# Performance work log

Hardware: AMD Instinct MI355X
Metric: run time of the kernel (lower is better)

The kernel has to match this reference:

```python
import jax, jax.numpy as jnp
import numpy as np


def setup_inputs() -> dict:
    key = jax.random.key(0)
    k1, k2, k3, k4 = jax.random.split(key, 4)
    T = 64            # decoder_batch_len (target steps)
    B = 32            # batch_size
    V = 50257         # decoder vocab size
    L = 400           # encoder (source) length
    rows = T * B
    vocab_ds = jax.random.uniform(k1, (rows, V), dtype=jnp.float32)
    attns = jax.random.uniform(k2, (rows, L), dtype=jnp.float32)
    p_gens = jax.random.uniform(k3, (rows, 1), dtype=jnp.float32)
    sources = jax.random.randint(k4, (L, B), 0, V, dtype=jnp.int64)
    return {
        "vocab_ds": vocab_ds,
        "attns": attns,
        "p_gens": p_gens,
        "sources": sources,
        "decoder_batch_len": T,
    }


def reference(vocab_ds, attns, p_gens, sources, decoder_batch_len):
    # vocab_ds: (T*B, V), attns: (T*B, L), p_gens: (T*B, 1), sources: (L, B)
    rows, V = vocab_ds.shape
    vocab_dists = p_gens * vocab_ds                      # gated generation dist
    attn_dists = (1.0 - p_gens) * attns                  # gated copy dist
    # sources.T tiled over decoder steps -> per-row vocab ids, shape (T*B, L)
    sources_rep = jnp.tile(sources.T, (decoder_batch_len, 1))
    row_idx = jnp.arange(rows)[:, None]                  # (T*B, 1) broadcasts over L
    # torch scatter_ (overwrite semantics) of copy probs into vocab slots
    attn_dists_projected = jnp.zeros((rows, V), dtype=vocab_ds.dtype).at[
        row_idx, sources_rep
    ].set(attn_dists, mode="drop")
    final_dists = attn_dists_projected + vocab_dists
    return final_dists
```

## Files before the change

kernel.cpp:

```cpp
#include <hip/hip_runtime.h>

__global__ __launch_bounds__(256) void distgen_kernel(
    const float* __restrict__ vocab_ds,
    const float* __restrict__ attns,
    const float* __restrict__ p_gens,
    const int*   __restrict__ sources,
    float* __restrict__ out,
    int V, int L, int B)
{
    const int row = blockIdx.x;
    const int tid = threadIdx.x;
    const size_t base = (size_t)row * (size_t)V;
    const float pg = p_gens[row];

    const int mis  = (int)(base & 3);
    const int pre  = mis ? (4 - mis) : 0;
    const int preN = pre < V ? pre : V;
    for (int j = tid; j < preN; j += blockDim.x)
        out[base + j] = pg * vocab_ds[base + j];

    const int rem  = V - preN;
    const int nvec = rem >> 2;
    const float4* __restrict__ v4 = (const float4*)(vocab_ds + base + preN);
    float4* __restrict__ o4       = (float4*)(out + base + preN);
    for (int i = tid; i < nvec; i += blockDim.x) {
        float4 x = v4[i];
        x.x *= pg; x.y *= pg; x.z *= pg; x.w *= pg;
        o4[i] = x;
    }
    for (int j = preN + (nvec << 2) + tid; j < V; j += blockDim.x)
        out[base + j] = pg * vocab_ds[base + j];

    __shared__ int s_src[512];
    const int b = row % B;
    const bool use_lds = (L <= 512);
    if (use_lds) {
        for (int l = tid; l < L; l += blockDim.x)
            s_src[l] = sources[(size_t)l * B + b];
    }
    __syncthreads();

    const float gate = 1.0f - pg;
    for (int l = tid; l < L; l += blockDim.x) {
        const int v = use_lds ? s_src[l] : sources[(size_t)l * B + b];
        if (v < 0 || v >= V) continue;
        bool last = true;
        if (use_lds) {
            for (int l2 = l + 1; l2 < L; ++l2)
                if (s_src[l2] == v) { last = false; break; }
        } else {
            for (int l2 = l + 1; l2 < L; ++l2)
                if (sources[(size_t)l2 * B + b] == v) { last = false; break; }
        }
        if (last) {
            const float a = gate * attns[(size_t)row * L + l];
            out[base + v] = pg * vocab_ds[base + v] + a;
        }
    }
}

extern "C" void kernel_launch(void* const* d_in, const int* in_sizes, int n_in,
                              void* d_out, int out_size, void* d_ws, size_t ws_size,
                              hipStream_t stream) {
    const float* vocab_ds = (const float*)d_in[0];
    const float* attns    = (const float*)d_in[1];
    const float* p_gens   = (const float*)d_in[2];
    const int*   sources  = (const int*)d_in[3];
    const int rows = in_sizes[2];
    const int V    = in_sizes[0] / rows;
    const int L    = in_sizes[1] / rows;
    const int B    = in_sizes[3] / L;
    float* out = (float*)d_out;

    distgen_kernel<<<rows, 256, 0, stream>>>(vocab_ds, attns, p_gens, sources,
                                             out, V, L, B);
}
```

Before: 282.5 us.

## Precompute per-batch last-occurrence mask and split into scale and scatter kernels

Moves the O(L^2) duplicate-source search out of every row into a small mask kernel that runs once per batch column and writes the surviving vocab ids to workspace. The main work then becomes a bandwidth-bound scale kernel (4x unrolled float4 loads, nontemporal stores) followed by a light scatter kernel that overwrites the copy positions. This removes the redundant per-row (T-fold) duplicate search and the latency it adds at the end of each block. In exchange it adds two launches and a second pass over roughly L scattered output elements per row, and it keeps the old fused kernel as a fallback when workspace is too small.

```diff
diff --git a/kernel.cpp b/kernel.cpp
--- a/kernel.cpp
+++ b/kernel.cpp
@@ -1,12 +1,96 @@
 #include <hip/hip_runtime.h>
 
-__global__ __launch_bounds__(256) void distgen_kernel(
-    const float* __restrict__ vocab_ds,
-    const float* __restrict__ attns,
-    const float* __restrict__ p_gens,
-    const int*   __restrict__ sources,
-    float* __restrict__ out,
-    int V, int L, int B)
+typedef float f32x4 __attribute__((ext_vector_type(4)));
+
+#define LMAX 1024
+
+__global__ __launch_bounds__(256) void mask_kernel(
+    const int* __restrict__ sources, int* __restrict__ vlast, int L, int B)
+{
+    const int b = blockIdx.x;
+    __shared__ int s_col[LMAX];
+    const bool use_lds = (L <= LMAX);
+    if (use_lds) {
+        for (int l = threadIdx.x; l < L; l += blockDim.x)
+            s_col[l] = sources[(size_t)l * B + b];
+    }
+    __syncthreads();
+    for (int l = threadIdx.x; l < L; l += blockDim.x) {
+        const int v = use_lds ? s_col[l] : sources[(size_t)l * B + b];
+        int keep = v;
+        if (use_lds) {
+            for (int l2 = l + 1; l2 < L; ++l2)
+                if (s_col[l2] == v) { keep = -1; break; }
+        } else {
+            for (int l2 = l + 1; l2 < L; ++l2)
+                if (sources[(size_t)l2 * B + b] == v) { keep = -1; break; }
+        }
+        vlast[(size_t)l * B + b] = keep;
+    }
+}
+
+__global__ __launch_bounds__(256) void scale_kernel(
+    const float* __restrict__ vd, const float* __restrict__ pgs,
+    float* __restrict__ out, int V)
+{
+    const int row = blockIdx.x;
+    const int tid = threadIdx.x;
+    const size_t base = (size_t)row * (size_t)V;
+    const float pg = pgs[row];
+
+    const int mis  = (int)(base & 3);
+    const int pre  = mis ? (4 - mis) : 0;
+    const int preN = pre < V ? pre : V;
+    for (int j = tid; j < preN; j += 256)
+        __builtin_nontemporal_store(pg * vd[base + j], &out[base + j]);
+
+    const int nvec = (V - preN) >> 2;
+    const f32x4* __restrict__ v4 = (const f32x4*)(vd + base + preN);
+    f32x4* __restrict__ o4       = (f32x4*)(out + base + preN);
+
+    int i = tid;
+    for (; i + 3 * 256 < nvec; i += 4 * 256) {
+        f32x4 a = v4[i];
+        f32x4 b = v4[i + 256];
+        f32x4 c = v4[i + 512];
+        f32x4 d = v4[i + 768];
+        a *= pg; b *= pg; c *= pg; d *= pg;
+        __builtin_nontemporal_store(a, &o4[i]);
+        __builtin_nontemporal_store(b, &o4[i + 256]);
+        __builtin_nontemporal_store(c, &o4[i + 512]);
+        __builtin_nontemporal_store(d, &o4[i + 768]);
+    }
+    for (; i < nvec; i += 256) {
+        f32x4 a = v4[i];
+        a *= pg;
+        __builtin_nontemporal_store(a, &o4[i]);
+    }
+    for (int j = preN + (nvec << 2) + tid; j < V; j += 256)
+        __builtin_nontemporal_store(pg * vd[base + j], &out[base + j]);
+}
+
+__global__ __launch_bounds__(128) void scatter_kernel(
+    const float* __restrict__ vd, const float* __restrict__ attns,
+    const float* __restrict__ pgs, const int* __restrict__ vlast,
+    float* __restrict__ out, int V, int L, int B)
+{
+    const int row = blockIdx.x;
+    const int b = row % B;
+    const float pg = pgs[row];
+    const float gate = 1.0f - pg;
+    const size_t base = (size_t)row * (size_t)V;
+    for (int l = threadIdx.x; l < L; l += 128) {
+        const int v = vlast[(size_t)l * B + b];
+        if (v >= 0 && v < V)
+            out[base + v] = fmaf(pg, vd[base + v],
+                                 gate * attns[(size_t)row * L + l]);
+    }
+}
+
+__global__ __launch_bounds__(256) void fused_fallback_kernel(
+    const float* __restrict__ vocab_ds, const float* __restrict__ attns,
+    const float* __restrict__ p_gens, const int* __restrict__ sources,
+    float* __restrict__ out, int V, int L, int B)
 {
     const int row = blockIdx.x;
     const int tid = threadIdx.x;
@@ -18,14 +102,12 @@
     const int preN = pre < V ? pre : V;
     for (int j = tid; j < preN; j += blockDim.x)
         out[base + j] = pg * vocab_ds[base + j];
-
-    const int rem  = V - preN;
-    const int nvec = rem >> 2;
-    const float4* __restrict__ v4 = (const float4*)(vocab_ds + base + preN);
-    float4* __restrict__ o4       = (float4*)(out + base + preN);
+    const int nvec = (V - preN) >> 2;
+    const f32x4* __restrict__ v4 = (const f32x4*)(vocab_ds + base + preN);
+    f32x4* __restrict__ o4       = (f32x4*)(out + base + preN);
     for (int i = tid; i < nvec; i += blockDim.x) {
-        float4 x = v4[i];
-        x.x *= pg; x.y *= pg; x.z *= pg; x.w *= pg;
+        f32x4 x = v4[i];
+        x *= pg;
         o4[i] = x;
     }
     for (int j = preN + (nvec << 2) + tid; j < V; j += blockDim.x)
@@ -39,18 +121,14 @@
             s_src[l] = sources[(size_t)l * B + b];
     }
     __syncthreads();
-
     const float gate = 1.0f - pg;
     for (int l = tid; l < L; l += blockDim.x) {
         const int v = use_lds ? s_src[l] : sources[(size_t)l * B + b];
         if (v < 0 || v >= V) continue;
         bool last = true;
-        if (use_lds) {
-            for (int l2 = l + 1; l2 < L; ++l2)
-                if (s_src[l2] == v) { last = false; break; }
-        } else {
-            for (int l2 = l + 1; l2 < L; ++l2)
-                if (sources[(size_t)l2 * B + b] == v) { last = false; break; }
+        for (int l2 = l + 1; l2 < L; ++l2) {
+            const int v2 = use_lds ? s_src[l2] : sources[(size_t)l2 * B + b];
+            if (v2 == v) { last = false; break; }
         }
         if (last) {
             const float a = gate * attns[(size_t)row * L + l];
@@ -72,6 +150,15 @@
     const int B    = in_sizes[3] / L;
     float* out = (float*)d_out;
 
-    distgen_kernel<<<rows, 256, 0, stream>>>(vocab_ds, attns, p_gens, sources,
-                                             out, V, L, B);
+    const size_t mask_bytes = (size_t)L * (size_t)B * sizeof(int);
+    if (ws_size >= mask_bytes) {
+        int* vlast = (int*)d_ws;
+        mask_kernel<<<B, 256, 0, stream>>>(sources, vlast, L, B);
+        scale_kernel<<<rows, 256, 0, stream>>>(vocab_ds, p_gens, out, V);
+        scatter_kernel<<<rows, 128, 0, stream>>>(vocab_ds, attns, p_gens,
+                                                 vlast, out, V, L, B);
+    } else {
+        fused_fallback_kernel<<<rows, 256, 0, stream>>>(
+            vocab_ds, attns, p_gens, sources, out, V, L, B);
+    }
 }
```

Result: faster. 248.6 us (-12.0%).

## Split into dedup prep, flat aligned scale pass, and sparse scatter-add kernels

Applied to the files above, without the earlier changes.

Replaces the per-row fused kernel with three kernels. A prep kernel deduplicates source ids per batch column once, using rank sort and keeping the last occurrence. A flat grid-stride kernel scales the whole vocab matrix with aligned 16-byte nontemporal stores, finding each element's row via magic-number division. A scatter kernel then adds the gated copy probabilities into the unique slots. This removes the per-row quadratic duplicate search and the misaligned row vectorisation. In exchange it adds two extra launches and a read-modify-write pass over the scattered output entries.

```diff
diff --git a/kernel.cpp b/kernel.cpp
--- a/kernel.cpp
+++ b/kernel.cpp
@@ -1,12 +1,134 @@
 #include <hip/hip_runtime.h>
 
-__global__ __launch_bounds__(256) void distgen_kernel(
-    const float* __restrict__ vocab_ds,
-    const float* __restrict__ attns,
-    const float* __restrict__ p_gens,
-    const int*   __restrict__ sources,
-    float* __restrict__ out,
-    int V, int L, int B)
+typedef float f32x4 __attribute__((ext_vector_type(4)));
+typedef unsigned int uint32;
+typedef unsigned long long uint64;
+
+#define LPAD 512
+#define LPG  4096
+
+__global__ __launch_bounds__(256) void prep_kernel(
+    const int* __restrict__ sources, int* __restrict__ uv, int* __restrict__ ul,
+    int* __restrict__ nu, int L, int B, int V)
+{
+    const int b = blockIdx.x;
+    __shared__ int s_col[LPAD];
+    __shared__ int s_sv[LPAD];
+    __shared__ int s_sl[LPAD];
+    __shared__ int s_cnt;
+    if (threadIdx.x == 0) s_cnt = 0;
+
+    for (int l = threadIdx.x; l < L; l += 256) {
+        const int v = sources[(size_t)l * B + b];
+        s_col[l] = (v >= 0 && v < V) ? v : 0x7FFFFFFF;
+    }
+    __syncthreads();
+
+    for (int l = threadIdx.x; l < L; l += 256) {
+        const int v = s_col[l];
+        int rank = 0;
+        for (int k = 0; k < L; ++k) {
+            const int vk = s_col[k];
+            rank += (vk < v) || (vk == v && k < l);
+        }
+        s_sv[rank] = v;
+        s_sl[rank] = l;
+    }
+    __syncthreads();
+
+    int* __restrict__ uvb = uv + (size_t)b * L;
+    int* __restrict__ ulb = ul + (size_t)b * L;
+    for (int t = threadIdx.x; t < L; t += 256) {
+        const int v = s_sv[t];
+        const bool surv = (v < V) && (t == L - 1 || s_sv[t + 1] != v);
+        if (surv) {
+            int pos = 0;
+            for (int k = 0; k < t; ++k) {
+                const int vk = s_sv[k];
+                pos += (vk < V) && (s_sv[k + 1] != vk);
+            }
+            uvb[pos] = v;
+            ulb[pos] = s_sl[t];
+            atomicAdd(&s_cnt, 1);
+        }
+    }
+    __syncthreads();
+    if (threadIdx.x == 0) nu[b] = s_cnt;
+}
+
+__global__ __launch_bounds__(256) void scale_flat_kernel(
+    const float* __restrict__ vd, const float* __restrict__ pgs,
+    float* __restrict__ out, int V, int rows,
+    uint64 magicM, long long ntiles, long long n4, long long total)
+{
+    __shared__ float s_pg[LPG];
+    for (int r = threadIdx.x; r < rows; r += 256) s_pg[r] = pgs[r];
+    __syncthreads();
+
+    const int tid = threadIdx.x;
+
+    for (long long s = blockIdx.x; s < ntiles; s += gridDim.x) {
+        const long long g = ((s << 8) + tid) << 2;
+        const uint32 row = (uint32)(((uint64)g * magicM) >> 48);
+        const uint32 j   = (uint32)((uint64)g - (uint64)row * (uint32)V);
+        f32x4 x = *(const f32x4*)(vd + g);
+        if (j + 4u <= (uint32)V) {
+            x *= s_pg[row];
+            __builtin_nontemporal_store(x, (f32x4*)(out + g));
+        } else {
+            f32x4 xo;
+#pragma unroll
+            for (int e = 0; e < 4; ++e) {
+                const uint32 re = (j + e >= (uint32)V) ? row + 1 : row;
+                xo[e] = x[e] * s_pg[re];
+            }
+            __builtin_nontemporal_store(xo, (f32x4*)(out + g));
+        }
+    }
+
+    for (long long i4 = (ntiles << 8) + (long long)blockIdx.x * 256 + tid;
+         i4 < n4; i4 += (long long)gridDim.x * 256) {
+        const long long g = i4 << 2;
+        const uint32 row = (uint32)(((uint64)g * magicM) >> 48);
+        const uint32 j   = (uint32)((uint64)g - (uint64)row * (uint32)V);
+        f32x4 x = *(const f32x4*)(vd + g);
+        f32x4 xo;
+#pragma unroll
+        for (int e = 0; e < 4; ++e) {
+            const uint32 re = (j + e >= (uint32)V) ? row + 1 : row;
+            xo[e] = x[e] * s_pg[re];
+        }
+        __builtin_nontemporal_store(xo, (f32x4*)(out + g));
+    }
+    for (long long g = (n4 << 2) + (long long)blockIdx.x * 256 + tid;
+         g < total; g += (long long)gridDim.x * 256) {
+        const uint32 row = (uint32)(((uint64)g * magicM) >> 48);
+        out[g] = s_pg[row] * vd[g];
+    }
+}
+
+__global__ __launch_bounds__(256) void scatter_add_kernel(
+    const float* __restrict__ attns, const float* __restrict__ pgs,
+    const int* __restrict__ uv, const int* __restrict__ ul,
+    const int* __restrict__ nu, float* __restrict__ out, int V, int L, int B)
+{
+    const int row = blockIdx.x;
+    const int b   = row % B;
+    const int n   = nu[b];
+    const float gate = 1.0f - pgs[row];
+    const size_t base = (size_t)row * (size_t)V;
+    const int* __restrict__ uvb = uv + (size_t)b * L;
+    const int* __restrict__ ulb = ul + (size_t)b * L;
+    for (int t = threadIdx.x; t < n; t += 256) {
+        const int v = uvb[t];
+        out[base + v] += gate * attns[(size_t)row * L + ulb[t]];
+    }
+}
+
+__global__ __launch_bounds__(256) void fused_fallback_kernel(
+    const float* __restrict__ vocab_ds, const float* __restrict__ attns,
+    const float* __restrict__ p_gens, const int* __restrict__ sources,
+    float* __restrict__ out, int V, int L, int B)
 {
     const int row = blockIdx.x;
     const int tid = threadIdx.x;
@@ -18,14 +140,12 @@
     const int preN = pre < V ? pre : V;
     for (int j = tid; j < preN; j += blockDim.x)
         out[base + j] = pg * vocab_ds[base + j];
-
-    const int rem  = V - preN;
-    const int nvec = rem >> 2;
-    const float4* __restrict__ v4 = (const float4*)(vocab_ds + base + preN);
-    float4* __restrict__ o4       = (float4*)(out + base + preN);
+    const int nvec = (V - preN) >> 2;
+    const f32x4* __restrict__ v4 = (const f32x4*)(vocab_ds + base + preN);
+    f32x4* __restrict__ o4       = (f32x4*)(out + base + preN);
     for (int i = tid; i < nvec; i += blockDim.x) {
-        float4 x = v4[i];
-        x.x *= pg; x.y *= pg; x.z *= pg; x.w *= pg;
+        f32x4 x = v4[i];
+        x *= pg;
         o4[i] = x;
     }
     for (int j = preN + (nvec << 2) + tid; j < V; j += blockDim.x)
@@ -39,18 +159,14 @@
             s_src[l] = sources[(size_t)l * B + b];
     }
     __syncthreads();
-
     const float gate = 1.0f - pg;
     for (int l = tid; l < L; l += blockDim.x) {
         const int v = use_lds ? s_src[l] : sources[(size_t)l * B + b];
         if (v < 0 || v >= V) continue;
         bool last = true;
-        if (use_lds) {
-            for (int l2 = l + 1; l2 < L; ++l2)
-                if (s_src[l2] == v) { last = false; break; }
-        } else {
-            for (int l2 = l + 1; l2 < L; ++l2)
-                if (sources[(size_t)l2 * B + b] == v) { last = false; break; }
+        for (int l2 = l + 1; l2 < L; ++l2) {
+            const int v2 = use_lds ? s_src[l2] : sources[(size_t)l2 * B + b];
+            if (v2 == v) { last = false; break; }
         }
         if (last) {
             const float a = gate * attns[(size_t)row * L + l];
@@ -72,6 +188,28 @@
     const int B    = in_sizes[3] / L;
     float* out = (float*)d_out;
 
-    distgen_kernel<<<rows, 256, 0, stream>>>(vocab_ds, attns, p_gens, sources,
-                                             out, V, L, B);
-}
+    const size_t need = (size_t)B * (size_t)L * 2 * sizeof(int)
+                      + (size_t)B * sizeof(int);
+    const bool fits = (ws_size >= need) && (L <= LPAD) && (rows <= LPG) &&
+                      ((long long)rows * V < (1ll << 40));
+    if (fits) {
+        int* uv = (int*)d_ws;
+        int* ul = uv + (size_t)B * (size_t)L;
+        int* nu = ul + (size_t)B * (size_t)L;
+
+        const long long total  = (long long)rows * (long long)V;
+        const long long n4     = total >> 2;
+        const long long ntiles = n4 >> 8;
+        const uint64 magicM =
+            (uint64)((((__uint128_t)1) << 48) / (uint32)V) + 1ull;
+
+        prep_kernel<<<B, 256, 0, stream>>>(sources, uv, ul, nu, L, B, V);
+        scale_flat_kernel<<<2048, 256, 0, stream>>>(
+            vocab_ds, p_gens, out, V, rows, magicM, ntiles, n4, total);
+        scatter_add_kernel<<<rows, 256, 0, stream>>>(
+            attns, p_gens, uv, ul, nu, out, V, L, B);
+    } else {
+        fused_fallback_kernel<<<rows, 256, 0, stream>>>(
+            vocab_ds, attns, p_gens, sources, out, V, L, B);
+    }
+}
```

After: 254.2 us. -10.0%, faster.
